# Kernel tuning notes

Hardware: AMD Instinct MI355X
Metric: run time of the kernel (lower is better)

## Reference

```python
import jax, jax.numpy as jnp
import numpy as np

BATCH = 2048
DIM = 1024       # discrete_dim
EMBED = 512
HID = 2 * EMBED  # MLP hidden width per source: [embed_dim*2, embed_dim*2, discrete_dim]
NUM_STEPS = 32


def setup_inputs() -> dict:
    key = jax.random.key(0)
    ks = jax.random.split(key, 8)
    s = 0.02  # init scale for weights
    init_samples = jax.random.randint(ks[0], (BATCH, DIM), 0, 2).astype(jnp.float32)
    target_pos = jax.random.randint(ks[1], (NUM_STEPS, BATCH), 0, DIM, dtype=jnp.int32)
    W1 = jax.random.normal(ks[2], (DIM, HID), jnp.float32) * s
    b1 = jnp.zeros((HID,), jnp.float32)
    W2 = jax.random.normal(ks[3], (HID, HID), jnp.float32) * s
    b2 = jnp.zeros((HID,), jnp.float32)
    W3 = jax.random.normal(ks[4], (HID, DIM), jnp.float32) * s
    b3 = jnp.zeros((DIM,), jnp.float32)
    return {
        "init_samples": init_samples, "target_pos": target_pos,
        "W1": W1, "b1": b1, "W2": W2, "b2": b2, "W3": W3, "b3": b3,
        "num_steps": NUM_STEPS,
    }


def _mlp(x, W1, b1, W2, b2, W3, b3):
    h = jax.nn.relu(x @ W1 + b1)
    h = jax.nn.relu(h @ W2 + b2)
    return h @ W3 + b3  # pos logits, [B, DIM]


def reference(init_samples, target_pos, W1, b1, W2, b2, W3, b3, num_steps):
    B = init_samples.shape[0]
    rows = jnp.arange(B)
    very_init_samples = init_samples
    total_log0 = jnp.zeros((B, 1), init_samples.dtype)  # mode != 'forward': total_log = 0.0

    def step(carry, tpos):
        samples, total_log = carry
        log_pos_prob = jax.nn.log_softmax(_mlp(samples, W1, b1, W2, b2, W3, b3), axis=-1)
        log_target = jnp.take_along_axis(log_pos_prob, tpos[:, None], axis=1)  # [B,1]
        total_log = total_log + log_target
        orig_bit = samples[rows, tpos]                       # gather, [B]
        samples = samples.at[rows, tpos].set(1.0 - orig_bit)  # scatter bit flip
        return (samples, total_log), tpos

    (final_samples, total_log), delta = jax.lax.scan(
        step, (init_samples, total_log0), target_pos[:num_steps])
    return final_samples, delta, total_log, very_init_samples
```

## Files before the change

### kernel.cpp

```cpp
#include <hip/hip_runtime.h>
#include <stdint.h>

#define BATCH 2048
#define NDIM  1024
#define HID   1024
#define TSTEPS 32

#define OUT_FINAL 0
#define OUT_DELTA 2097152
#define OUT_TOTAL 2162688
#define OUT_VINIT 2164736

#define SC_ROWSUM 0
#define SC_TGT    8192
#define SC_TOTAL  16384
#define SC_BIAS   24576
#define SC_FLAG   36864

#define WF_WT1    0u
#define WF_WT2    2097152u
#define WF_WT3    4194304u
#define WF_A1     6291456u
#define WF_BIAS   14680064u
#define WF_SIGNS  14692352u
#define WF_ROWSUM 14757888u
#define WF_TGT    15020032u
#define WF_FLAG   15282176u
#define WF_H1     15286272u

__device__ __forceinline__ float bf2f(ushort u) {
  union { uint32_t u; float f; } v; v.u = ((uint32_t)u) << 16; return v.f;
}
__device__ __forceinline__ ushort f2bf(float f) {
  union { float f; uint32_t u; } v; v.f = f;
  uint32_t u = v.u;
  u += 0x7fffu + ((u >> 16) & 1u);
  return (ushort)(u >> 16);
}

typedef __attribute__((ext_vector_type(8))) short bf16x8;
typedef __attribute__((ext_vector_type(8))) unsigned short u16x8;
typedef __attribute__((ext_vector_type(4))) float f32x4;

__device__ __forceinline__ void gload_lds16(const void* g, void* l) {
  __builtin_amdgcn_global_load_lds((const __attribute__((address_space(1))) void*)g,
                                   (__attribute__((address_space(3))) void*)l, 16, 0, 0);
}

__global__ __launch_bounds__(256) void flag_k(const void* __restrict__ init,
                                              uint32_t* __restrict__ flag) {
  const ushort* p = (const ushort*)init;
  __shared__ uint32_t acc[256];
  uint32_t a = 0;
  for (int i = threadIdx.x; i < 32768; i += 256) a |= p[2 * i];
  acc[threadIdx.x] = a;
  __syncthreads();
  for (int s = 128; s > 0; s >>= 1) {
    if (threadIdx.x < s) acc[threadIdx.x] |= acc[threadIdx.x + s];
    __syncthreads();
  }
  if (threadIdx.x == 0) *flag = (acc[0] != 0) ? 1u : 0u;
}

__global__ __launch_bounds__(256) void zero_k(float* __restrict__ p) {
  p[blockIdx.x * 256 + threadIdx.x] = 0.f;
}

__global__ __launch_bounds__(256) void canon_b_k(const void* b1, const void* b2,
                                                 const void* b3,
                                                 float* __restrict__ dst,
                                                 const uint32_t* __restrict__ flag) {
  const void* src = (blockIdx.x == 0) ? b1 : (blockIdx.x == 1) ? b2 : b3;
  float* d = dst + blockIdx.x * 1024;
  const bool isbf = (*flag != 0);
  for (int i = threadIdx.x; i < 1024; i += 256)
    d[i] = isbf ? bf2f(((const ushort*)src)[i]) : ((const float*)src)[i];
}

__global__ __launch_bounds__(256) void canon_w3_k(const void* __restrict__ S1,
                                                  const void* __restrict__ S2,
                                                  const void* __restrict__ S3,
                                                  ushort* __restrict__ D,
                                                  const uint32_t* __restrict__ flag) {
  __shared__ ushort tile[32][33];
  const void* S = (blockIdx.z == 0) ? S1 : (blockIdx.z == 1) ? S2 : S3;
  ushort* Dz = D + (size_t)blockIdx.z * 1024 * 1024;
  const int bx = blockIdx.x * 32, by = blockIdx.y * 32;
  const int tx = threadIdx.x, ty = threadIdx.y;
  const bool isbf = (*flag != 0);
  #pragma unroll
  for (int i = 0; i < 32; i += 8) {
    const size_t idx = (size_t)(by + ty + i) * 1024 + bx + tx;
    tile[ty + i][tx] = isbf ? ((const ushort*)S)[idx] : f2bf(((const float*)S)[idx]);
  }
  __syncthreads();
  #pragma unroll
  for (int i = 0; i < 32; i += 8)
    Dz[(size_t)(bx + ty + i) * 1024 + by + tx] = tile[tx][ty + i];
}

__global__ __launch_bounds__(256) void sign_k(const void* __restrict__ init,
                                              const int* __restrict__ tpos,
                                              uint8_t* __restrict__ signs,
                                              const uint32_t* __restrict__ flag) {
  const int m = blockIdx.x, tid = threadIdx.x;
  const bool isbf = (*flag != 0);
  __shared__ float bits[NDIM];
  #pragma unroll
  for (int i = 0; i < 4; ++i) {
    const int k = tid + i * 256;
    bits[k] = isbf ? bf2f(((const ushort*)init)[(size_t)m * NDIM + k])
                   : ((const float*)init)[(size_t)m * NDIM + k];
  }
  __syncthreads();
  if (tid == 0) {
    for (int t = 0; t < TSTEPS; ++t) {
      const int tp = tpos[t * BATCH + m];
      const float b = bits[tp];
      signs[t * BATCH + m] = (uint8_t)(b != 0.f);
      bits[tp] = 1.f - b;
    }
  }
}

template <int ASTAGE, int EPI>
__global__ __launch_bounds__(256) void gemm_bt(const void* __restrict__ A,
                                               const ushort* __restrict__ Bt,
                                               const float* __restrict__ bias,
                                               void* __restrict__ Cout,
                                               const int* __restrict__ tpos,
                                               float* __restrict__ rowsum,
                                               float* __restrict__ tgt,
                                               const uint32_t* __restrict__ flag,
                                               int rowbase) {
  constexpr int BM = 128, BN = 128, BK = 64, K = 1024;
  __shared__ ushort Asm[BM * BK];
  __shared__ ushort Bsm[BN * BK];
  const int tid = threadIdx.x;
  const int wave = tid >> 6, lane = tid & 63;
  const int q = lane >> 4, r = lane & 15;

  const int lid = blockIdx.y * gridDim.x + blockIdx.x;
  const int xcd = lid & 7;
  const int sl  = lid >> 3;
  const int mb  = xcd + 8 * (sl >> 3);
  const int nb  = sl & 7;
  const int n0 = nb * BN;
  const int m0 = mb * BM;
  const int wm = (wave & 1) * 64, wn = (wave >> 1) * 64;

  f32x4 acc[4][4];
  #pragma unroll
  for (int i = 0; i < 4; ++i)
    #pragma unroll
    for (int j = 0; j < 4; ++j)
      #pragma unroll
      for (int e = 0; e < 4; ++e) acc[i][j][e] = 0.f;

  int srow[4], ssrc[4], sdst[4];
  #pragma unroll
  for (int j = 0; j < 4; ++j) {
    const int f = j * 4096 + tid * 16;
    const int rw = f >> 7;
    const int c  = (f & 127) >> 4;
    srow[j] = rw;
    ssrc[j] = (c ^ (rw & 7)) * 8;
    sdst[j] = f;
  }
  const bool isbf = (ASTAGE == 1) ? (*flag != 0) : true;

  for (int k0 = 0; k0 < K; k0 += BK) {
    if constexpr (ASTAGE == 0) {
      #pragma unroll
      for (int j = 0; j < 4; ++j)
        gload_lds16((const char*)A + ((size_t)(m0 + srow[j]) * K + k0 + ssrc[j]) * 2,
                    (char*)Asm + sdst[j]);
    } else {
      u16x8 avv[4];
      #pragma unroll
      for (int j = 0; j < 4; ++j) {
        if (isbf) {
          avv[j] = *(const u16x8*)((const ushort*)A + (size_t)(m0 + srow[j]) * K + k0 + ssrc[j]);
        } else {
          const float* fp = (const float*)A + (size_t)(m0 + srow[j]) * K + k0 + ssrc[j];
          const float4 fa = *(const float4*)fp, fb = *(const float4*)(fp + 4);
          avv[j][0] = f2bf(fa.x); avv[j][1] = f2bf(fa.y); avv[j][2] = f2bf(fa.z); avv[j][3] = f2bf(fa.w);
          avv[j][4] = f2bf(fb.x); avv[j][5] = f2bf(fb.y); avv[j][6] = f2bf(fb.z); avv[j][7] = f2bf(fb.w);
        }
      }
      #pragma unroll
      for (int j = 0; j < 4; ++j) *(u16x8*)((char*)Asm + sdst[j]) = avv[j];
    }
    #pragma unroll
    for (int j = 0; j < 4; ++j)
      gload_lds16((const char*)Bt + ((size_t)(n0 + srow[j]) * K + k0 + ssrc[j]) * 2,
                  (char*)Bsm + sdst[j]);
    __syncthreads();
    #pragma unroll
    for (int s = 0; s < 2; ++s) {
      bf16x8 af[4], bfr[4];
      #pragma unroll
      for (int t = 0; t < 4; ++t) {
        const int ra = wm + t * 16 + r;
        af[t]  = *(const bf16x8*)(Asm + ra * BK + (((s * 4 + q) ^ (ra & 7)) * 8));
        const int rb = wn + t * 16 + r;
        bfr[t] = *(const bf16x8*)(Bsm + rb * BK + (((s * 4 + q) ^ (rb & 7)) * 8));
      }
      #pragma unroll
      for (int mt = 0; mt < 4; ++mt)
        #pragma unroll
        for (int nt = 0; nt < 4; ++nt)
          acc[mt][nt] = __builtin_amdgcn_mfma_f32_16x16x32_bf16(af[mt], bfr[nt], acc[mt][nt], 0, 0, 0);
    }
    __syncthreads();
  }

  #pragma unroll
  for (int mt = 0; mt < 4; ++mt) {
    #pragma unroll
    for (int reg = 0; reg < 4; ++reg) {
      const int grow = m0 + wm + mt * 16 + q * 4 + reg;
      if constexpr (EPI == 2) {
        const int growg = rowbase + grow;
        const int tp = tpos[growg];
        float s2 = 0.f;
        #pragma unroll
        for (int nt = 0; nt < 4; ++nt) {
          const int gcol = n0 + wn + nt * 16 + r;
          const float v = acc[mt][nt][reg] + bias[gcol];
          if (gcol == tp) tgt[growg] = v;
          s2 += __expf(v);
        }
        s2 += __shfl_xor(s2, 1);
        s2 += __shfl_xor(s2, 2);
        s2 += __shfl_xor(s2, 4);
        s2 += __shfl_xor(s2, 8);
        if (r == 0) atomicAdd(&rowsum[growg], s2);
      } else {
        #pragma unroll
        for (int nt = 0; nt < 4; ++nt) {
          const int gcol = n0 + wn + nt * 16 + r;
          const float v = acc[mt][nt][reg] + bias[gcol];
          if constexpr (EPI == 0) {
            ((float*)Cout)[(size_t)grow * NDIM + gcol] = v;
          } else {
            ((ushort*)Cout)[(size_t)grow * NDIM + gcol] = f2bf(v > 0.f ? v : 0.f);
          }
        }
      }
    }
  }
}

__global__ __launch_bounds__(256) void build_h1(float* __restrict__ a1,
                                                const void* __restrict__ W1,
                                                const uint8_t* __restrict__ signs,
                                                const int* __restrict__ tpos,
                                                ushort* __restrict__ h1,
                                                const uint32_t* __restrict__ flag,
                                                int t0, int nsteps) {
  const int m = blockIdx.x;
  const int k = threadIdx.x * 4;
  const bool isbf = (*flag != 0);
  float4 a = *(const float4*)(a1 + (size_t)m * HID + k);
  for (int t = 0; t < nsteps; ++t) {
    ushort4 h;
    h.x = f2bf(a.x > 0.f ? a.x : 0.f);
    h.y = f2bf(a.y > 0.f ? a.y : 0.f);
    h.z = f2bf(a.z > 0.f ? a.z : 0.f);
    h.w = f2bf(a.w > 0.f ? a.w : 0.f);
    *(ushort4*)(h1 + ((size_t)(t * BATCH + m)) * HID + k) = h;
    const int tg = t0 + t;
    const int tp = tpos[tg * BATCH + m];
    const float s = 1.f - 2.f * (float)signs[tg * BATCH + m];
    float wx, wy, wz, ww;
    if (isbf) {
      const ushort4 wv = *(const ushort4*)((const ushort*)W1 + (size_t)tp * HID + k);
      wx = bf2f(wv.x); wy = bf2f(wv.y); wz = bf2f(wv.z); ww = bf2f(wv.w);
    } else {
      const float4 wv = *(const float4*)((const float*)W1 + (size_t)tp * HID + k);
      wx = wv.x; wy = wv.y; wz = wv.z; ww = wv.w;
    }
    a.x += s * wx; a.y += s * wy; a.z += s * wz; a.w += s * ww;
  }
  *(float4*)(a1 + (size_t)m * HID + k) = a;
}

__global__ __launch_bounds__(256) void fin_total_k(const float* __restrict__ tgt,
                                                   const float* __restrict__ rowsum,
                                                   float* __restrict__ out_total) {
  const int m = blockIdx.x * 256 + threadIdx.x;
  float acc = 0.f;
  for (int t = 0; t < TSTEPS; ++t) {
    const int rr = t * BATCH + m;
    acc += tgt[rr] - logf(rowsum[rr]);
  }
  out_total[m] = acc;
}

template <int ASRC, int EPI>
__global__ __launch_bounds__(256) void gemm_t(const void* __restrict__ A,
                                              const void* __restrict__ W,
                                              const float* __restrict__ bias,
                                              ushort* __restrict__ Cout,
                                              const int* __restrict__ tpos,
                                              float* __restrict__ rowsum,
                                              float* __restrict__ tgt,
                                              const uint32_t* __restrict__ flag,
                                              int tstep) {
  constexpr int BM = 64, BN = 64, BK = 32, BKP = 40, K = 1024;
  __shared__ ushort Asm[BM * BKP];
  __shared__ ushort Bsm[BN * BKP];
  const int tid = threadIdx.x;
  const int w = tid >> 6, lane = tid & 63;
  const int q = lane >> 4, r = lane & 15;
  const int n0 = blockIdx.x * BN;
  const int m0 = blockIdx.y * BM;
  const bool isbf = (*flag != 0);
  const int srow = tid >> 2, scol = (tid & 3) * 8;
  const int kk = tid >> 3, ng = (tid & 7) * 8;

  f32x4 acc[4];
  #pragma unroll
  for (int nt = 0; nt < 4; ++nt)
    #pragma unroll
    for (int e = 0; e < 4; ++e) acc[nt][e] = 0.f;

  for (int k0 = 0; k0 < K; k0 += BK) {
    u16x8 av;
    if constexpr (ASRC == 0) {
      if (isbf) {
        av = *(const u16x8*)((const ushort*)A + (size_t)(m0 + srow) * K + k0 + scol);
      } else {
        const float* fp = (const float*)A + (size_t)(m0 + srow) * K + k0 + scol;
        const float4 fa = *(const float4*)fp, fb = *(const float4*)(fp + 4);
        av[0] = f2bf(fa.x); av[1] = f2bf(fa.y); av[2] = f2bf(fa.z); av[3] = f2bf(fa.w);
        av[4] = f2bf(fb.x); av[5] = f2bf(fb.y); av[6] = f2bf(fb.z); av[7] = f2bf(fb.w);
      }
    } else {
      av = *(const u16x8*)((const ushort*)A + (size_t)(m0 + srow) * K + k0 + scol);
      if constexpr (ASRC == 1) {
        #pragma unroll
        for (int e = 0; e < 8; ++e) av[e] = (av[e] & 0x8000u) ? (unsigned short)0 : av[e];
      }
    }
    ushort bw[8];
    if (isbf) {
      const u16x8 wv = *(const u16x8*)((const ushort*)W + (size_t)(k0 + kk) * NDIM + n0 + ng);
      #pragma unroll
      for (int j = 0; j < 8; ++j) bw[j] = wv[j];
    } else {
      const float* fp = (const float*)W + (size_t)(k0 + kk) * NDIM + n0 + ng;
      const float4 fa = *(const float4*)fp, fb = *(const float4*)(fp + 4);
      bw[0] = f2bf(fa.x); bw[1] = f2bf(fa.y); bw[2] = f2bf(fa.z); bw[3] = f2bf(fa.w);
      bw[4] = f2bf(fb.x); bw[5] = f2bf(fb.y); bw[6] = f2bf(fb.z); bw[7] = f2bf(fb.w);
    }
    __syncthreads();
    *(u16x8*)(Asm + srow * BKP + scol) = av;
    #pragma unroll
    for (int j = 0; j < 8; ++j) Bsm[(ng + j) * BKP + kk] = bw[j];
    __syncthreads();
    const bf16x8 af = *(const bf16x8*)(Asm + (w * 16 + r) * BKP + q * 8);
    #pragma unroll
    for (int nt = 0; nt < 4; ++nt) {
      const bf16x8 bfr = *(const bf16x8*)(Bsm + (nt * 16 + r) * BKP + q * 8);
      acc[nt] = __builtin_amdgcn_mfma_f32_16x16x32_bf16(af, bfr, acc[nt], 0, 0, 0);
    }
  }

  if constexpr (EPI == 2) {
    #pragma unroll
    for (int reg = 0; reg < 4; ++reg) {
      const int grow = m0 + w * 16 + q * 4 + reg;
      const int tp = tpos[tstep * BATCH + grow];
      float s = 0.f;
      #pragma unroll
      for (int nt = 0; nt < 4; ++nt) {
        const int gcol = n0 + nt * 16 + r;
        const float v = acc[nt][reg] + bias[gcol];
        if (gcol == tp) tgt[grow] = v;
        s += __expf(v);
      }
      s += __shfl_xor(s, 1);
      s += __shfl_xor(s, 2);
      s += __shfl_xor(s, 4);
      s += __shfl_xor(s, 8);
      if (r == 0) atomicAdd(&rowsum[grow], s);
    }
  } else {
    #pragma unroll
    for (int nt = 0; nt < 4; ++nt) {
      #pragma unroll
      for (int reg = 0; reg < 4; ++reg) {
        const int grow = m0 + w * 16 + q * 4 + reg;
        const int gcol = n0 + nt * 16 + r;
        float v = acc[nt][reg] + bias[gcol];
        if constexpr (EPI == 1) v = (v > 0.f) ? v : 0.f;
        Cout[(size_t)grow * NDIM + gcol] = f2bf(v);
      }
    }
  }
}

__global__ __launch_bounds__(256) void step_k(ushort* __restrict__ a1,
                                              const void* __restrict__ init,
                                              const void* __restrict__ W1,
                                              const int* __restrict__ tpos,
                                              float* __restrict__ rowsum,
                                              const float* __restrict__ tgt,
                                              float* __restrict__ total,
                                              const uint32_t* __restrict__ flag,
                                              int t) {
  const int m = blockIdx.x;
  const int k = threadIdx.x * 4;
  const bool isbf = (*flag != 0);
  const int tp = tpos[t * BATCH + m];
  const float b0 = isbf ? bf2f(((const ushort*)init)[(size_t)m * NDIM + tp])
                        : ((const float*)init)[(size_t)m * NDIM + tp];
  int cnt = 0;
  for (int u = 0; u < t; ++u) cnt += (tpos[u * BATCH + m] == tp) ? 1 : 0;
  const float bit = (cnt & 1) ? (1.f - b0) : b0;
  const float s = 1.f - 2.f * bit;
  float wx, wy, wz, ww;
  if (isbf) {
    const ushort4 wv = *(const ushort4*)((const ushort*)W1 + (size_t)tp * HID + k);
    wx = bf2f(wv.x); wy = bf2f(wv.y); wz = bf2f(wv.z); ww = bf2f(wv.w);
  } else {
    const float4 wv = *(const float4*)((const float*)W1 + (size_t)tp * HID + k);
    wx = wv.x; wy = wv.y; wz = wv.z; ww = wv.w;
  }
  ushort4 a = *(const ushort4*)(a1 + (size_t)m * HID + k);
  a.x = f2bf(bf2f(a.x) + s * wx);
  a.y = f2bf(bf2f(a.y) + s * wy);
  a.z = f2bf(bf2f(a.z) + s * wz);
  a.w = f2bf(bf2f(a.w) + s * ww);
  *(ushort4*)(a1 + (size_t)m * HID + k) = a;
  if (threadIdx.x == 0) {
    total[m] += tgt[m] - logf(rowsum[m]);
    rowsum[m] = 0.f;
  }
}

__global__ __launch_bounds__(256) void finalize_k(const float* __restrict__ total,
                                                  float* __restrict__ out_total) {
  const int m = blockIdx.x * 256 + threadIdx.x;
  out_total[m] = total[m];
}

__global__ __launch_bounds__(256) void out_final_k(const void* __restrict__ init,
                                                   const int* __restrict__ tpos,
                                                   float* __restrict__ out,
                                                   const uint32_t* __restrict__ flag) {
  const int m = blockIdx.x;
  const int k = threadIdx.x * 4;
  const bool isbf = (*flag != 0);
  float v[4];
  if (isbf) {
    const ushort4 iv = *(const ushort4*)((const ushort*)init + (size_t)m * NDIM + k);
    v[0] = bf2f(iv.x); v[1] = bf2f(iv.y); v[2] = bf2f(iv.z); v[3] = bf2f(iv.w);
  } else {
    const float4 iv = *(const float4*)((const float*)init + (size_t)m * NDIM + k);
    v[0] = iv.x; v[1] = iv.y; v[2] = iv.z; v[3] = iv.w;
  }
  for (int t = 0; t < TSTEPS; ++t) {
    const int tp = tpos[t * BATCH + m];
    if ((tp >> 2) == (int)threadIdx.x) v[tp & 3] = 1.f - v[tp & 3];
  }
  float4 o; o.x = v[0]; o.y = v[1]; o.z = v[2]; o.w = v[3];
  *(float4*)(out + OUT_FINAL + (size_t)m * NDIM + k) = o;
}

__global__ __launch_bounds__(256) void out_vinit_k(const void* __restrict__ init,
                                                   float* __restrict__ out,
                                                   const uint32_t* __restrict__ flag) {
  const int i = (blockIdx.x * 256 + threadIdx.x) * 4;
  float4 o;
  if (*flag) {
    const ushort4 iv = *(const ushort4*)((const ushort*)init + i);
    o.x = bf2f(iv.x); o.y = bf2f(iv.y); o.z = bf2f(iv.z); o.w = bf2f(iv.w);
  } else {
    o = *(const float4*)((const float*)init + i);
  }
  *(float4*)(out + OUT_VINIT + i) = o;
}

__global__ __launch_bounds__(256) void out_delta_k(const int* __restrict__ tpos,
                                                   float* __restrict__ out) {
  const int i = blockIdx.x * 256 + threadIdx.x;
  out[OUT_DELTA + i] = (float)tpos[i];
}

extern "C" void kernel_launch(void* const* d_in, const int* in_sizes, int n_in,
                              void* d_out, int out_size, void* d_ws, size_t ws_size,
                              hipStream_t stream) {
  const void* init = d_in[0];
  const int* tpos  = (const int*)d_in[1];
  const void* W1 = d_in[2];
  const void* b1 = d_in[3];
  const void* W2 = d_in[4];
  const void* b2 = d_in[5];
  const void* W3 = d_in[6];
  const void* b3 = d_in[7];
  float* out = (float*)d_out;
  char* ws = (char*)d_ws;

  const size_t MB = 1024ull * 1024ull;
  int CH = TSTEPS;
  while (CH > 1 && (size_t)WF_H1 + (size_t)CH * 8 * MB > ws_size) CH >>= 1;
  const bool fast = (ws_size >= (size_t)WF_H1 + 8 * MB);

  if (fast) {
    ushort*   WT1    = (ushort*)(ws + WF_WT1);
    ushort*   WT2    = (ushort*)(ws + WF_WT2);
    ushort*   WT3    = (ushort*)(ws + WF_WT3);
    float*    a1f    = (float*)(ws + WF_A1);
    float*    biases = (float*)(ws + WF_BIAS);
    uint8_t*  signs  = (uint8_t*)(ws + WF_SIGNS);
    float*    rowsum = (float*)(ws + WF_ROWSUM);
    float*    tgt    = (float*)(ws + WF_TGT);
    uint32_t* flag   = (uint32_t*)(ws + WF_FLAG);
    ushort*   h1     = (ushort*)(ws + WF_H1);
    ushort*   h2     = (ushort*)(ws + WF_H1 + (size_t)CH * 4 * MB);

    flag_k<<<1, 256, 0, stream>>>(init, flag);
    canon_b_k<<<3, 256, 0, stream>>>(b1, b2, b3, biases, flag);
    canon_w3_k<<<dim3(32, 32, 3), dim3(32, 8), 0, stream>>>(W1, W2, W3, WT1, flag);
    sign_k<<<BATCH, 256, 0, stream>>>(init, tpos, signs, flag);
    zero_k<<<512, 256, 0, stream>>>(rowsum);

    gemm_bt<1, 0><<<dim3(8, 16), 256, 0, stream>>>(init, WT1, biases + 0, a1f,
                                                   nullptr, nullptr, nullptr, flag, 0);

    for (int t0 = 0; t0 < TSTEPS; t0 += CH) {
      build_h1<<<BATCH, 256, 0, stream>>>(a1f, W1, signs, tpos, h1, flag, t0, CH);
      gemm_bt<0, 1><<<dim3(8, CH * 16), 256, 0, stream>>>(h1, WT2, biases + 1024, h2,
                                                          nullptr, nullptr, nullptr, flag, 0);
      gemm_bt<0, 2><<<dim3(8, CH * 16), 256, 0, stream>>>(h2, WT3, biases + 2048, nullptr,
                                                          tpos, rowsum, tgt, flag, t0 * BATCH);
    }
    fin_total_k<<<8, 256, 0, stream>>>(tgt, rowsum, out + OUT_TOTAL);
    out_final_k<<<BATCH, 256, 0, stream>>>(init, tpos, out, flag);
    out_vinit_k<<<2048, 256, 0, stream>>>(init, out, flag);
    out_delta_k<<<256, 256, 0, stream>>>(tpos, out);
  } else {
    ushort*   a1     = (ushort*)(out + OUT_FINAL);
    ushort*   h2     = (ushort*)(out + OUT_VINIT);
    char*     sc     = (char*)(out + OUT_DELTA);
    float*    rowsum = (float*)(sc + SC_ROWSUM);
    float*    tgt    = (float*)(sc + SC_TGT);
    float*    total  = (float*)(sc + SC_TOTAL);
    float*    biases = (float*)(sc + SC_BIAS);
    uint32_t* flag   = (uint32_t*)(sc + SC_FLAG);

    flag_k<<<1, 256, 0, stream>>>(init, flag);
    zero_k<<<24, 256, 0, stream>>>(rowsum);
    canon_b_k<<<3, 256, 0, stream>>>(b1, b2, b3, biases, flag);
    gemm_t<0, 0><<<dim3(16, 32), 256, 0, stream>>>(init, W1, biases + 0, a1,
                                                   nullptr, nullptr, nullptr, flag, 0);
    for (int t = 0; t < TSTEPS; ++t) {
      gemm_t<1, 1><<<dim3(16, 32), 256, 0, stream>>>(a1, W2, biases + 1024, h2,
                                                     nullptr, nullptr, nullptr, flag, 0);
      gemm_t<2, 2><<<dim3(16, 32), 256, 0, stream>>>(h2, W3, biases + 2048, nullptr,
                                                     tpos, rowsum, tgt, flag, t);
      step_k<<<BATCH, 256, 0, stream>>>(a1, init, W1, tpos, rowsum, tgt, total, flag, t);
    }
    finalize_k<<<8, 256, 0, stream>>>(total, out + OUT_TOTAL);
    out_final_k<<<BATCH, 256, 0, stream>>>(init, tpos, out, flag);
    out_vinit_k<<<2048, 256, 0, stream>>>(init, out, flag);
    out_delta_k<<<256, 256, 0, stream>>>(tpos, out);
  }
}
```

Baseline: 592.7 us.

## Register-prefetch GEMM main loop, fuse zeroing and output kernels

The bf16 MFMA GEMM main loop changes from direct global-to-LDS loads over 64-wide K tiles with an XOR swizzle to a register-prefetched pipeline. It now uses 32-wide K tiles and a padded LDS row stride, so the next tile's global loads overlap the current tile's MFMAs. The accumulator zeroing moves into sign_k, and the four output kernels (total, final samples, initial copy, delta) merge into one per-row kernel. This cuts launch count, but gives up the asynchronous LDS load path and doubles the number of barrier pairs per K extent.

```diff
diff --git a/kernel.cpp b/kernel.cpp
--- a/kernel.cpp
+++ b/kernel.cpp
@@ -41,11 +41,6 @@
 typedef __attribute__((ext_vector_type(8))) short bf16x8;
 typedef __attribute__((ext_vector_type(8))) unsigned short u16x8;
 typedef __attribute__((ext_vector_type(4))) float f32x4;
-
-__device__ __forceinline__ void gload_lds16(const void* g, void* l) {
-  __builtin_amdgcn_global_load_lds((const __attribute__((address_space(1))) void*)g,
-                                   (__attribute__((address_space(3))) void*)l, 16, 0, 0);
-}
 
 __global__ __launch_bounds__(256) void flag_k(const void* __restrict__ init,
                                               uint32_t* __restrict__ flag) {
@@ -102,6 +97,8 @@
 __global__ __launch_bounds__(256) void sign_k(const void* __restrict__ init,
                                               const int* __restrict__ tpos,
                                               uint8_t* __restrict__ signs,
+                                              float* __restrict__ rowsum,
+                                              float* __restrict__ tgt,
                                               const uint32_t* __restrict__ flag) {
   const int m = blockIdx.x, tid = threadIdx.x;
   const bool isbf = (*flag != 0);
@@ -121,6 +118,8 @@
       bits[tp] = 1.f - b;
     }
   }
+  if (tid < 32) rowsum[m * 32 + tid] = 0.f;
+  else if (tid < 64) tgt[m * 32 + (tid - 32)] = 0.f;
 }
 
 template <int ASTAGE, int EPI>
@@ -133,9 +132,9 @@
                                                float* __restrict__ tgt,
                                                const uint32_t* __restrict__ flag,
                                                int rowbase) {
-  constexpr int BM = 128, BN = 128, BK = 64, K = 1024;
-  __shared__ ushort Asm[BM * BK];
-  __shared__ ushort Bsm[BN * BK];
+  constexpr int BM = 128, BN = 128, BK = 32, LS = 40, K = 1024;
+  __shared__ ushort Asm[BM * LS];
+  __shared__ ushort Bsm[BN * LS];
   const int tid = threadIdx.x;
   const int wave = tid >> 6, lane = tid & 63;
   const int q = lane >> 4, r = lane & 15;
@@ -157,62 +156,74 @@
       #pragma unroll
       for (int e = 0; e < 4; ++e) acc[i][j][e] = 0.f;
 
-  int srow[4], ssrc[4], sdst[4];
-  #pragma unroll
-  for (int j = 0; j < 4; ++j) {
-    const int f = j * 4096 + tid * 16;
-    const int rw = f >> 7;
-    const int c  = (f & 127) >> 4;
-    srow[j] = rw;
-    ssrc[j] = (c ^ (rw & 7)) * 8;
-    sdst[j] = f;
-  }
+  const int row = tid >> 2, c8 = (tid & 3) * 8;
   const bool isbf = (ASTAGE == 1) ? (*flag != 0) : true;
 
+  u16x8 pa0, pa1, pb0, pb1;
+  {
+    if constexpr (ASTAGE == 1) {
+      if (isbf) {
+        pa0 = *(const u16x8*)((const ushort*)A + (size_t)(m0 + row) * K + c8);
+        pa1 = *(const u16x8*)((const ushort*)A + (size_t)(m0 + 64 + row) * K + c8);
+      } else {
+        const float* p0 = (const float*)A + (size_t)(m0 + row) * K + c8;
+        const float* p1 = (const float*)A + (size_t)(m0 + 64 + row) * K + c8;
+        const float4 fa = *(const float4*)p0, fb = *(const float4*)(p0 + 4);
+        const float4 fc = *(const float4*)p1, fd = *(const float4*)(p1 + 4);
+        pa0[0] = f2bf(fa.x); pa0[1] = f2bf(fa.y); pa0[2] = f2bf(fa.z); pa0[3] = f2bf(fa.w);
+        pa0[4] = f2bf(fb.x); pa0[5] = f2bf(fb.y); pa0[6] = f2bf(fb.z); pa0[7] = f2bf(fb.w);
+        pa1[0] = f2bf(fc.x); pa1[1] = f2bf(fc.y); pa1[2] = f2bf(fc.z); pa1[3] = f2bf(fc.w);
+        pa1[4] = f2bf(fd.x); pa1[5] = f2bf(fd.y); pa1[6] = f2bf(fd.z); pa1[7] = f2bf(fd.w);
+      }
+    } else {
+      pa0 = *(const u16x8*)((const ushort*)A + (size_t)(m0 + row) * K + c8);
+      pa1 = *(const u16x8*)((const ushort*)A + (size_t)(m0 + 64 + row) * K + c8);
+    }
+    pb0 = *(const u16x8*)(Bt + (size_t)(n0 + row) * K + c8);
+    pb1 = *(const u16x8*)(Bt + (size_t)(n0 + 64 + row) * K + c8);
+  }
+
   for (int k0 = 0; k0 < K; k0 += BK) {
-    if constexpr (ASTAGE == 0) {
+    __syncthreads();
+    *(u16x8*)(Asm + row * LS + c8) = pa0;
+    *(u16x8*)(Asm + (64 + row) * LS + c8) = pa1;
+    *(u16x8*)(Bsm + row * LS + c8) = pb0;
+    *(u16x8*)(Bsm + (64 + row) * LS + c8) = pb1;
+    {
+      const int kn = (k0 + BK) & (K - 1);
+      if constexpr (ASTAGE == 1) {
+        if (isbf) {
+          pa0 = *(const u16x8*)((const ushort*)A + (size_t)(m0 + row) * K + kn + c8);
+          pa1 = *(const u16x8*)((const ushort*)A + (size_t)(m0 + 64 + row) * K + kn + c8);
+        } else {
+          const float* p0 = (const float*)A + (size_t)(m0 + row) * K + kn + c8;
+          const float* p1 = (const float*)A + (size_t)(m0 + 64 + row) * K + kn + c8;
+          const float4 fa = *(const float4*)p0, fb = *(const float4*)(p0 + 4);
+          const float4 fc = *(const float4*)p1, fd = *(const float4*)(p1 + 4);
+          pa0[0] = f2bf(fa.x); pa0[1] = f2bf(fa.y); pa0[2] = f2bf(fa.z); pa0[3] = f2bf(fa.w);
+          pa0[4] = f2bf(fb.x); pa0[5] = f2bf(fb.y); pa0[6] = f2bf(fb.z); pa0[7] = f2bf(fb.w);
+          pa1[0] = f2bf(fc.x); pa1[1] = f2bf(fc.y); pa1[2] = f2bf(fc.z); pa1[3] = f2bf(fc.w);
+          pa1[4] = f2bf(fd.x); pa1[5] = f2bf(fd.y); pa1[6] = f2bf(fd.z); pa1[7] = f2bf(fd.w);
+        }
+      } else {
+        pa0 = *(const u16x8*)((const ushort*)A + (size_t)(m0 + row) * K + kn + c8);
+        pa1 = *(const u16x8*)((const ushort*)A + (size_t)(m0 + 64 + row) * K + kn + c8);
+      }
+      pb0 = *(const u16x8*)(Bt + (size_t)(n0 + row) * K + kn + c8);
+      pb1 = *(const u16x8*)(Bt + (size_t)(n0 + 64 + row) * K + kn + c8);
+    }
+    __syncthreads();
+    bf16x8 af[4], bfr[4];
+    #pragma unroll
+    for (int t = 0; t < 4; ++t) {
+      af[t]  = *(const bf16x8*)(Asm + (wm + t * 16 + r) * LS + q * 8);
+      bfr[t] = *(const bf16x8*)(Bsm + (wn + t * 16 + r) * LS + q * 8);
+    }
+    #pragma unroll
+    for (int mt = 0; mt < 4; ++mt)
       #pragma unroll
-      for (int j = 0; j < 4; ++j)
-        gload_lds16((const char*)A + ((size_t)(m0 + srow[j]) * K + k0 + ssrc[j]) * 2,
-                    (char*)Asm + sdst[j]);
-    } else {
-      u16x8 avv[4];
-      #pragma unroll
-      for (int j = 0; j < 4; ++j) {
-        if (isbf) {
-          avv[j] = *(const u16x8*)((const ushort*)A + (size_t)(m0 + srow[j]) * K + k0 + ssrc[j]);
-        } else {
-          const float* fp = (const float*)A + (size_t)(m0 + srow[j]) * K + k0 + ssrc[j];
-          const float4 fa = *(const float4*)fp, fb = *(const float4*)(fp + 4);
-          avv[j][0] = f2bf(fa.x); avv[j][1] = f2bf(fa.y); avv[j][2] = f2bf(fa.z); avv[j][3] = f2bf(fa.w);
-          avv[j][4] = f2bf(fb.x); avv[j][5] = f2bf(fb.y); avv[j][6] = f2bf(fb.z); avv[j][7] = f2bf(fb.w);
-        }
-      }
-      #pragma unroll
-      for (int j = 0; j < 4; ++j) *(u16x8*)((char*)Asm + sdst[j]) = avv[j];
-    }
-    #pragma unroll
-    for (int j = 0; j < 4; ++j)
-      gload_lds16((const char*)Bt + ((size_t)(n0 + srow[j]) * K + k0 + ssrc[j]) * 2,
-                  (char*)Bsm + sdst[j]);
-    __syncthreads();
-    #pragma unroll
-    for (int s = 0; s < 2; ++s) {
-      bf16x8 af[4], bfr[4];
-      #pragma unroll
-      for (int t = 0; t < 4; ++t) {
-        const int ra = wm + t * 16 + r;
-        af[t]  = *(const bf16x8*)(Asm + ra * BK + (((s * 4 + q) ^ (ra & 7)) * 8));
-        const int rb = wn + t * 16 + r;
-        bfr[t] = *(const bf16x8*)(Bsm + rb * BK + (((s * 4 + q) ^ (rb & 7)) * 8));
-      }
-      #pragma unroll
-      for (int mt = 0; mt < 4; ++mt)
-        #pragma unroll
-        for (int nt = 0; nt < 4; ++nt)
-          acc[mt][nt] = __builtin_amdgcn_mfma_f32_16x16x32_bf16(af[mt], bfr[nt], acc[mt][nt], 0, 0, 0);
-    }
-    __syncthreads();
+      for (int nt = 0; nt < 4; ++nt)
+        acc[mt][nt] = __builtin_amdgcn_mfma_f32_16x16x32_bf16(af[mt], bfr[nt], acc[mt][nt], 0, 0, 0);
   }
 
   #pragma unroll
@@ -286,16 +297,43 @@
   *(float4*)(a1 + (size_t)m * HID + k) = a;
 }
 
-__global__ __launch_bounds__(256) void fin_total_k(const float* __restrict__ tgt,
-                                                   const float* __restrict__ rowsum,
-                                                   float* __restrict__ out_total) {
-  const int m = blockIdx.x * 256 + threadIdx.x;
-  float acc = 0.f;
+__global__ __launch_bounds__(256) void outputs_k(const void* __restrict__ init,
+                                                 const int* __restrict__ tpos,
+                                                 const float* __restrict__ tgt,
+                                                 const float* __restrict__ rowsum,
+                                                 float* __restrict__ out,
+                                                 const uint32_t* __restrict__ flag) {
+  const int m = blockIdx.x;
+  const int tid = threadIdx.x;
+  const int k = tid * 4;
+  const bool isbf = (*flag != 0);
+  float v[4];
+  if (isbf) {
+    const ushort4 iv = *(const ushort4*)((const ushort*)init + (size_t)m * NDIM + k);
+    v[0] = bf2f(iv.x); v[1] = bf2f(iv.y); v[2] = bf2f(iv.z); v[3] = bf2f(iv.w);
+  } else {
+    const float4 iv = *(const float4*)((const float*)init + (size_t)m * NDIM + k);
+    v[0] = iv.x; v[1] = iv.y; v[2] = iv.z; v[3] = iv.w;
+  }
+  float4 o0; o0.x = v[0]; o0.y = v[1]; o0.z = v[2]; o0.w = v[3];
+  *(float4*)(out + OUT_VINIT + (size_t)m * NDIM + k) = o0;
   for (int t = 0; t < TSTEPS; ++t) {
-    const int rr = t * BATCH + m;
-    acc += tgt[rr] - logf(rowsum[rr]);
-  }
-  out_total[m] = acc;
+    const int tp = tpos[t * BATCH + m];
+    if ((tp >> 2) == tid) v[tp & 3] = 1.f - v[tp & 3];
+  }
+  float4 o; o.x = v[0]; o.y = v[1]; o.z = v[2]; o.w = v[3];
+  *(float4*)(out + OUT_FINAL + (size_t)m * NDIM + k) = o;
+  if (tid < 32) out[OUT_DELTA + m * 32 + tid] = (float)tpos[m * 32 + tid];
+  if (tid < 64) {
+    const int t = tid & 31;
+    float s = tgt[t * BATCH + m] - logf(rowsum[t * BATCH + m]);
+    s += __shfl_xor(s, 1, 32);
+    s += __shfl_xor(s, 2, 32);
+    s += __shfl_xor(s, 4, 32);
+    s += __shfl_xor(s, 8, 32);
+    s += __shfl_xor(s, 16, 32);
+    if (tid == 0) out[OUT_TOTAL + m] = s;
+  }
 }
 
 template <int ASRC, int EPI>
@@ -525,8 +563,7 @@
     flag_k<<<1, 256, 0, stream>>>(init, flag);
     canon_b_k<<<3, 256, 0, stream>>>(b1, b2, b3, biases, flag);
     canon_w3_k<<<dim3(32, 32, 3), dim3(32, 8), 0, stream>>>(W1, W2, W3, WT1, flag);
-    sign_k<<<BATCH, 256, 0, stream>>>(init, tpos, signs, flag);
-    zero_k<<<512, 256, 0, stream>>>(rowsum);
+    sign_k<<<BATCH, 256, 0, stream>>>(init, tpos, signs, rowsum, tgt, flag);
 
     gemm_bt<1, 0><<<dim3(8, 16), 256, 0, stream>>>(init, WT1, biases + 0, a1f,
                                                    nullptr, nullptr, nullptr, flag, 0);
@@ -538,10 +575,7 @@
       gemm_bt<0, 2><<<dim3(8, CH * 16), 256, 0, stream>>>(h2, WT3, biases + 2048, nullptr,
                                                           tpos, rowsum, tgt, flag, t0 * BATCH);
     }
-    fin_total_k<<<8, 256, 0, stream>>>(tgt, rowsum, out + OUT_TOTAL);
-    out_final_k<<<BATCH, 256, 0, stream>>>(init, tpos, out, flag);
-    out_vinit_k<<<2048, 256, 0, stream>>>(init, out, flag);
-    out_delta_k<<<256, 256, 0, stream>>>(tpos, out);
+    outputs_k<<<BATCH, 256, 0, stream>>>(init, tpos, tgt, rowsum, out, flag);
   } else {
     ushort*   a1     = (ushort*)(out + OUT_FINAL);
     ushort*   h2     = (ushort*)(out + OUT_VINIT);
```

Result: no change. 592.0 us (-0.1%).
